# Performance work log

Hardware: AMD Instinct MI355X
Metric: run time of the kernel (lower is better)

The kernel has to match this reference:

```python
import jax, jax.numpy as jnp
import numpy as np

B, S, D_MODEL, D_MEM, N_HEADS, NU = 8, 2048, 1024, 1024, 16, 3
D_HEAD = D_MODEL // N_HEADS            # 64
D_KEY = 2 * NU * (D_MEM // N_HEADS)    # 384


def _to_heads(x, n_heads):
    b, s, d = x.shape
    return x.reshape(b, s, n_heads, d // n_heads).transpose(0, 2, 1, 3)


def _dpfp(x, nu):
    # Deterministic Positive Feature Projection: (..., d) -> (..., 2*nu*d)
    x = jnp.concatenate([jax.nn.relu(x), jax.nn.relu(-x)], axis=-1)
    rolled = jnp.concatenate([jnp.roll(x, j, axis=-1) for j in range(1, nu + 1)], axis=-1)
    rep = jnp.concatenate([x] * nu, axis=-1)
    return rep * rolled


def setup_inputs() -> dict:
    key = jax.random.key(0)
    k0, k1, k2, k3, k4 = jax.random.split(key, 5)
    mem_tokens = jax.random.normal(k0, (B, S, D_MODEL), dtype=jnp.float32)
    # nn.Linear(in, out) weight shape is [out, in]
    W_mk = jax.random.normal(k1, (D_MEM, D_MODEL), dtype=jnp.float32) * 0.02
    W_mv = jax.random.normal(k2, (D_MODEL, D_MODEL), dtype=jnp.float32) * 0.02
    W_mb = jax.random.normal(k3, (D_MODEL, D_MODEL), dtype=jnp.float32) * 0.02
    W_mem = jax.random.normal(k4, (B, N_HEADS, D_KEY, D_HEAD), dtype=jnp.float32) * 0.01
    z = jnp.ones((B, N_HEADS, D_KEY), dtype=jnp.float32)
    return {"mem_tokens": mem_tokens, "W_mk": W_mk, "W_mv": W_mv, "W_mb": W_mb,
            "W_mem": W_mem, "z": z}


def reference(mem_tokens, W_mk, W_mv, W_mb, W_mem, z):
    # key projection + DPFP feature map
    k = _to_heads(mem_tokens @ W_mk.T, N_HEADS)          # [b,h,s,d_mem/h]
    mk = _dpfp(k, NU)                                     # [b,h,s,d_key]
    norm = jnp.linalg.norm(mk, axis=-1, keepdims=True)
    mk = mk / jnp.maximum(norm, 1e-12)                    # F.normalize(p=2)

    new_mv = _to_heads(mem_tokens @ W_mv.T, N_HEADS)      # [b,h,s,d_head]

    # retrieve previous values (first_seg=False, use_denom=True path)
    num = jnp.einsum('bhsk,bhkd->bhsd', mk, W_mem)
    denom = jnp.einsum('bhk,bhsk->bhs', z, mk)[..., None] + 1e-5
    prev_mv = num / denom

    mv = new_mv - prev_mv
    mb = _to_heads(jax.nn.sigmoid(mem_tokens @ W_mb.T), N_HEADS)

    # gating=True einsum: 'ihjk,ihjt,ihjt->ihkt'
    associations = jnp.einsum('bhsk,bhsd,bhsd->bhkd', mk, mv, mb)
    return W_mem + associations
```

## Files before the change

kernel.cpp:

```cpp
#include <hip/hip_runtime.h>
#include <hip/hip_bf16.h>

#define B_ 8
#define S_ 2048
#define DM 1024
#define H_ 16
#define DH 64
#define DK 384

#define AS3 __attribute__((address_space(3)))
#define AS1 __attribute__((address_space(1)))
typedef unsigned int u32;

typedef __attribute__((ext_vector_type(8))) short bf16x8;
typedef __attribute__((ext_vector_type(4))) short bf16x4;
typedef __attribute__((ext_vector_type(4))) float f32x4;

static __device__ __forceinline__ ushort f2b(float f) {
  __hip_bfloat16 h = __float2bfloat16(f);
  return *reinterpret_cast<ushort*>(&h);
}
static __device__ __forceinline__ float b2f(ushort u) {
  __hip_bfloat16 h;
  *reinterpret_cast<ushort*>(&h) = u;
  return __bfloat162float(h);
}

__global__ __launch_bounds__(256) void k_cvt(
    const float* __restrict__ X, const float* __restrict__ Wk,
    const float* __restrict__ Wv, const float* __restrict__ Wb,
    ushort* __restrict__ Xb, ushort* __restrict__ Wball) {
  const int total = 2097152 + 3 * 131072;
  int c = blockIdx.x * 256 + threadIdx.x;
  const int stride = gridDim.x * 256;
  for (; c < total; c += stride) {
    const float* s;
    ushort* d;
    size_t off;
    if (c < 2097152) { s = X; d = Xb; off = (size_t)c; }
    else {
      int cc = c - 2097152;
      int wsel = cc >> 17;
      off = (size_t)(cc & 131071);
      s = wsel == 0 ? Wk : (wsel == 1 ? Wv : Wb);
      d = Wball + (size_t)wsel * (DM * DM);
    }
    float4 a = *(const float4*)(s + off * 8);
    float4 b = *(const float4*)(s + off * 8 + 4);
    ushort u[8] = { f2b(a.x), f2b(a.y), f2b(a.z), f2b(a.w),
                    f2b(b.x), f2b(b.y), f2b(b.z), f2b(b.w) };
    *(uint4*)(d + off * 8) = *(uint4*)u;
  }
}

__global__ __launch_bounds__(256) void k_proj(
    const ushort* __restrict__ Xb, const ushort* __restrict__ Wball,
    ushort* __restrict__ kvb) {
  __shared__ ushort SH[17408];
  ushort* As = SH;
  ushort* Bs = SH + 8192;
  const int t = threadIdx.x, lane = t & 63, w = t >> 6;
  const int wm = w >> 1, wn = w & 1;
  const int l15 = lane & 15, lq = lane >> 4;
  const int bid = blockIdx.x + (blockIdx.y << 7) + (blockIdx.z << 10);
  const int c = bid & 7, r = bid >> 3;
  const int zb = r >> 7;
  const int rem = r & 127;
  const int mgrp = rem >> 3;
  const int nb = rem & 7;
  const int m0 = (c * 16 + mgrp) * 128;
  const int n0 = nb * 128;
  const int wsel = zb;
  const ushort* Wmat = Wball + (size_t)wsel * (DM * DM);
  ushort* out = kvb + (size_t)wsel * ((size_t)B_ * H_ * S_ * DH);

  auto STAGE = [&](int buf, int k0) {
    #pragma unroll
    for (int j = 0; j < 2; j++) {
      int row = (t >> 2) + j * 64;
      int col8 = (t & 3) * 8;
      __builtin_amdgcn_global_load_lds(
          (const AS1 u32*)(Xb + (size_t)(m0 + row) * DM + k0 + col8),
          (AS3 u32*)(As + buf * 4096 + j * 2048 + t * 8), 16, 0, 0);
      __builtin_amdgcn_global_load_lds(
          (const AS1 u32*)(Wmat + (size_t)(n0 + row) * DM + k0 + col8),
          (AS3 u32*)(Bs + buf * 4096 + j * 2048 + t * 8), 16, 0, 0);
    }
  };

  f32x4 acc[4][4] = {};
  STAGE(0, 0);
  __syncthreads();
  int cur = 0;
  for (int kt = 0; kt < 32; kt++) {
    if (kt < 31) STAGE(cur ^ 1, (kt + 1) * 32);
    const ushort* Ab = As + cur * 4096;
    const ushort* Bb = Bs + cur * 4096;
    bf16x8 af[4], bfr[4];
    #pragma unroll
    for (int mi = 0; mi < 4; mi++)
      af[mi] = *(const bf16x8*)&Ab[(wm * 64 + mi * 16 + l15) * 32 + lq * 8];
    #pragma unroll
    for (int ni = 0; ni < 4; ni++)
      bfr[ni] = *(const bf16x8*)&Bb[(wn * 64 + ni * 16 + l15) * 32 + lq * 8];
    #pragma unroll
    for (int mi = 0; mi < 4; mi++)
      #pragma unroll
      for (int ni = 0; ni < 4; ni++)
        acc[mi][ni] = __builtin_amdgcn_mfma_f32_16x16x32_bf16(af[mi], bfr[ni], acc[mi][ni], 0, 0, 0);
    __syncthreads();
    cur ^= 1;
  }

  ushort (*Cb)[136] = (ushort (*)[136])SH;
  #pragma unroll
  for (int mi = 0; mi < 4; mi++)
    #pragma unroll
    for (int ni = 0; ni < 4; ni++)
      #pragma unroll
      for (int rr = 0; rr < 4; rr++) {
        float val = acc[mi][ni][rr];
        if (wsel == 2) val = 1.0f / (1.0f + __expf(-val));
        Cb[wm * 64 + mi * 16 + lq * 4 + rr][wn * 64 + ni * 16 + l15] = f2b(val);
      }
  __syncthreads();
  #pragma unroll
  for (int q = 0; q < 8; q++) {
    int idx = q * 256 + t;
    int lm = idx >> 4;
    int c16 = idx & 15;
    int m = m0 + lm;
    int b = m >> 11, s = m & 2047;
    int o0 = n0 + c16 * 8;
    int h = o0 >> 6, d = o0 & 63;
    *(uint4*)(out + (((size_t)(b * H_ + h)) * S_ + s) * DH + d) =
        *(uint4*)&Cb[lm][c16 * 8];
  }
}

__global__ __launch_bounds__(512) void k_fused6(
    const ushort* __restrict__ Kb, const ushort* __restrict__ Vb,
    const ushort* __restrict__ Bgb, const float* __restrict__ Wmem,
    const float* __restrict__ z, ushort* __restrict__ part) {
  __shared__ u32 mkLd[32][192];
  __shared__ ushort mkT[384][36];
  __shared__ ushort gLT[64][36];
  __shared__ ushort zL[384];
  const int t = threadIdx.x, l = t & 63, w = t >> 6;
  const int l15 = l & 15, lq = l >> 4;
  const int bh = blockIdx.y, seg = blockIdx.x;
  const size_t rowbase = (size_t)bh * S_;
  const int mi = w >> 2, ni = w & 3;
  const int dcol = ni * 16 + l15;

  for (int cc = t; cc < DK; cc += 512) {
    int u = cc >> 7, p = (cc & 127) >> 1, par = cc & 1;
    zL[cc] = f2b(z[(size_t)bh * DK + u * 128 + par * 64 + p]);
  }

  const float* Wm = Wmem + (size_t)bh * (DK * DH);
  bf16x8 bw[12];
  #pragma unroll
  for (int k0i = 0; k0i < 12; k0i++) {
    bf16x8 tmp;
    #pragma unroll
    for (int j = 0; j < 8; j++) {
      int cc = k0i * 32 + lq * 8 + j;
      int u = cc >> 7, p = (cc & 127) >> 1, par = cc & 1;
      tmp[j] = (short)f2b(Wm[(size_t)(u * 128 + par * 64 + p) * DH + dcol]);
    }
    bw[k0i] = tmp;
  }

  f32x4 acc[3][4] = {};
  ushort kreg[4], vreg[4], breg[4];

  auto LOADCH = [&](int ch) {
    const int s0 = seg * 512 + ch * 32;
    #pragma unroll
    for (int r = 0; r < 4; r++)
      kreg[r] = Kb[(rowbase + s0 + w * 4 + r) * DH + l];
    #pragma unroll
    for (int rr = 0; rr < 4; rr++) {
      size_t ga = (rowbase + s0 + mi * 16 + lq * 4 + rr) * DH + dcol;
      vreg[rr] = Vb[ga];
      breg[rr] = Bgb[ga];
    }
  };

  LOADCH(0);
  __syncthreads();

  for (int ch = 0; ch < 16; ch++) {
    float xpv[4], xnv[4];
    u32 pks[4];
    #pragma unroll
    for (int r = 0; r < 4; r++) {
      float kv = b2f(kreg[r]);
      xpv[r] = fmaxf(kv, 0.f);
      xnv[r] = fmaxf(-kv, 0.f);
      pks[r] = (u32)f2b(xpv[r]) | ((u32)f2b(xnv[r]) << 16);
    }
    ushort4 mp[6];
    #pragma unroll
    for (int u = 0; u < 3; u++) {
      int ie = (l - u - 1) & 127;
      int sl = ie & 63;
      bool sw = ie >= 64;
      #pragma unroll
      for (int r = 0; r < 4; r++) {
        u32 pp = (u32)__shfl((int)pks[r], sl);
        float ps = b2f((ushort)(pp & 0xffff));
        float ns = b2f((ushort)(pp >> 16));
        float xbe = sw ? ns : ps;
        float xbo = sw ? ps : ns;
        ushort bve = f2b(xpv[r] * xbe);
        ushort bvo = f2b(xnv[r] * xbo);
        int row = w * 4 + r;
        mkLd[row][(u * 64 + l) ^ ((row & 7) << 2)] = (u32)bve | ((u32)bvo << 16);
        ((ushort*)&mp[2 * u])[r] = bve;
        ((ushort*)&mp[2 * u + 1])[r] = bvo;
      }
    }
    #pragma unroll
    for (int tt = 0; tt < 6; tt++)
      *(ushort4*)&mkT[l + 64 * tt][w * 4] = mp[tt];
    __syncthreads();

    const u32* mkrow = &mkLd[mi * 16 + l15][0];
    const int xr = (l15 & 7) << 2;
    f32x4 an0 = {}, an1 = {}, gacc = {}, zacc = {};
    #pragma unroll
    for (int k0i = 0; k0i < 12; k0i += 2) {
      bf16x8 afA = *(const bf16x8*)(mkrow + ((k0i * 16 + lq * 4) ^ xr));
      bf16x8 afB = *(const bf16x8*)(mkrow + (((k0i + 1) * 16 + lq * 4) ^ xr));
      bf16x8 zfA = *(const bf16x8*)&zL[k0i * 32 + lq * 8];
      bf16x8 zfB = *(const bf16x8*)&zL[(k0i + 1) * 32 + lq * 8];
      an0 = __builtin_amdgcn_mfma_f32_16x16x32_bf16(afA, bw[k0i], an0, 0, 0, 0);
      an1 = __builtin_amdgcn_mfma_f32_16x16x32_bf16(afB, bw[k0i + 1], an1, 0, 0, 0);
      gacc = __builtin_amdgcn_mfma_f32_16x16x32_bf16(afA, afA, gacc, 0, 0, 0);
      gacc = __builtin_amdgcn_mfma_f32_16x16x32_bf16(afB, afB, gacc, 0, 0, 0);
      zacc = __builtin_amdgcn_mfma_f32_16x16x32_bf16(afA, zfA, zacc, 0, 0, 0);
      zacc = __builtin_amdgcn_mfma_f32_16x16x32_bf16(afB, zfB, zacc, 0, 0, 0);
    }
    f32x4 an = an0 + an1;
    float ssqv[4];
    #pragma unroll
    for (int rr = 0; rr < 4; rr++)
      ssqv[rr] = __shfl(gacc[rr], (lq << 4) + lq * 4 + rr);
    {
      ushort4 gp;
      #pragma unroll
      for (int rr = 0; rr < 4; rr++) {
        float inv = 1.0f / fmaxf(sqrtf(ssqv[rr]), 1e-12f);
        float rden = 1.0f / (inv * zacc[rr] + 1e-5f);
        float prev = an[rr] * inv * rden;
        float g = (b2f(vreg[rr]) - prev) * b2f(breg[rr]);
        ((ushort*)&gp)[rr] = f2b(g * inv);
      }
      *(ushort4*)&gLT[dcol][mi * 16 + lq * 4] = gp;
    }
    __syncthreads();

    if (ch < 15) LOADCH(ch + 1);

    {
      bf16x8 bfr[4];
      #pragma unroll
      for (int n2 = 0; n2 < 4; n2++) {
        bf16x4 blo = *(const bf16x4*)&gLT[n2 * 16 + l15][lq * 8];
        bf16x4 bhi = *(const bf16x4*)&gLT[n2 * 16 + l15][lq * 8 + 4];
        bfr[n2] = __builtin_shufflevector(blo, bhi, 0, 1, 2, 3, 4, 5, 6, 7);
      }
      #pragma unroll
      for (int m2 = 0; m2 < 3; m2++) {
        bf16x4 alo = *(const bf16x4*)&mkT[w * 48 + m2 * 16 + l15][lq * 8];
        bf16x4 ahi = *(const bf16x4*)&mkT[w * 48 + m2 * 16 + l15][lq * 8 + 4];
        bf16x8 af = __builtin_shufflevector(alo, ahi, 0, 1, 2, 3, 4, 5, 6, 7);
        #pragma unroll
        for (int n2 = 0; n2 < 4; n2++)
          acc[m2][n2] = __builtin_amdgcn_mfma_f32_16x16x32_bf16(af, bfr[n2], acc[m2][n2], 0, 0, 0);
      }
    }
    __syncthreads();
  }

  ushort* pb = part + ((size_t)bh * 4 + seg) * (DK * DH);
  #pragma unroll
  for (int m2 = 0; m2 < 3; m2++)
    #pragma unroll
    for (int n2 = 0; n2 < 4; n2++)
      #pragma unroll
      for (int rc = 0; rc < 4; rc++)
        pb[(size_t)(w * 48 + m2 * 16 + lq * 4 + rc) * DH + n2 * 16 + l15] =
            f2b(acc[m2][n2][rc]);
}

__global__ __launch_bounds__(256) void k_reduce(
    const float* __restrict__ Wmem, const ushort* __restrict__ part,
    float* __restrict__ out) {
  size_t i4 = (size_t)blockIdx.x * 256 + threadIdx.x;
  int bh = (int)(i4 / 6144);
  size_t r4 = i4 - (size_t)bh * 6144;
  float4 acc = *(const float4*)(Wmem + i4 * 4);
  #pragma unroll
  for (int k = 0; k < 4; k++) {
    const ushort* pp = part + ((size_t)bh * 4 + k) * (DK * DH) + r4 * 4;
    ushort4 pv = *(const ushort4*)pp;
    acc.x += b2f(pv.x);
    acc.y += b2f(pv.y);
    acc.z += b2f(pv.z);
    acc.w += b2f(pv.w);
  }
  *(float4*)(out + i4 * 4) = acc;
}

extern "C" void kernel_launch(void* const* d_in, const int* in_sizes, int n_in,
                              void* d_out, int out_size, void* d_ws, size_t ws_size,
                              hipStream_t stream) {
  const float* X  = (const float*)d_in[0];
  const float* Wk = (const float*)d_in[1];
  const float* Wv = (const float*)d_in[2];
  const float* Wb = (const float*)d_in[3];
  const float* Wm = (const float*)d_in[4];
  const float* z  = (const float*)d_in[5];
  float* out = (float*)d_out;
  char* ws = (char*)d_ws;

  ushort* Xb    = (ushort*)(ws);
  ushort* Wball = (ushort*)(ws + 33554432ull);
  ushort* kvb   = (ushort*)(ws + 39845888ull);
  ushort* part  = (ushort*)(ws);
  ushort* Kb  = kvb;
  ushort* Vb  = kvb + (size_t)B_ * H_ * S_ * DH;
  ushort* Bgb = kvb + 2ull * (size_t)B_ * H_ * S_ * DH;

  k_cvt   <<<dim3(2048), 256, 0, stream>>>(X, Wk, Wv, Wb, Xb, Wball);
  k_proj  <<<dim3(128, 8, 3), 256, 0, stream>>>(Xb, Wball, kvb);
  k_fused6<<<dim3(4, B_ * H_), 512, 0, stream>>>(Kb, Vb, Bgb, Wm, z, part);
  k_reduce<<<dim3(3072), 256, 0, stream>>>(Wm, part, out);
}
```

Baseline: 274.4 us.

## Double K-tile depth and XOR-swizzle LDS layout in projection GEMM

The projection GEMM now stages 64-wide K tiles instead of 32, halving the number of loop iterations and barriers. Global-to-LDS loads use an XOR swizzle on the 16-byte column chunks to avoid LDS bank conflicts on the fragment reads, and the row pointers are precomputed. The main loop is fully unrolled. LDS use grows to 64 KB per block, which may reduce occupancy.

```diff
diff --git a/kernel.cpp b/kernel.cpp
--- a/kernel.cpp
+++ b/kernel.cpp
@@ -56,9 +56,7 @@
 __global__ __launch_bounds__(256) void k_proj(
     const ushort* __restrict__ Xb, const ushort* __restrict__ Wball,
     ushort* __restrict__ kvb) {
-  __shared__ ushort SH[17408];
-  ushort* As = SH;
-  ushort* Bs = SH + 8192;
+  __shared__ ushort SH[4 * 8192];
   const int t = threadIdx.x, lane = t & 63, w = t >> 6;
   const int wm = w >> 1, wn = w & 1;
   const int l15 = lane & 15, lq = lane >> 4;
@@ -74,42 +72,62 @@
   const ushort* Wmat = Wball + (size_t)wsel * (DM * DM);
   ushort* out = kvb + (size_t)wsel * ((size_t)B_ * H_ * S_ * DH);
 
-  auto STAGE = [&](int buf, int k0) {
-    #pragma unroll
-    for (int j = 0; j < 2; j++) {
-      int row = (t >> 2) + j * 64;
-      int col8 = (t & 3) * 8;
+  const int rowst = (lane >> 3);
+  const int colsw = ((lane & 7) ^ rowst) << 3;
+
+  const ushort* pX[4];
+  const ushort* pW[4];
+  #pragma unroll
+  for (int j = 0; j < 4; j++) {
+    int row = (w * 4 + j) * 8 + rowst;
+    pX[j] = Xb + (size_t)(m0 + row) * DM + colsw;
+    pW[j] = Wmat + (size_t)(n0 + row) * DM + colsw;
+  }
+  ushort* dA = SH + w * 2048;
+  ushort* dB = SH + 16384 + w * 2048;
+
+  auto STAGE = [&](int buf, int kidx) {
+    #pragma unroll
+    for (int j = 0; j < 4; j++) {
       __builtin_amdgcn_global_load_lds(
-          (const AS1 u32*)(Xb + (size_t)(m0 + row) * DM + k0 + col8),
-          (AS3 u32*)(As + buf * 4096 + j * 2048 + t * 8), 16, 0, 0);
+          (const AS1 u32*)(pX[j] + kidx * 64),
+          (AS3 u32*)(dA + buf * 8192 + j * 512), 16, 0, 0);
       __builtin_amdgcn_global_load_lds(
-          (const AS1 u32*)(Wmat + (size_t)(n0 + row) * DM + k0 + col8),
-          (AS3 u32*)(Bs + buf * 4096 + j * 2048 + t * 8), 16, 0, 0);
+          (const AS1 u32*)(pW[j] + kidx * 64),
+          (AS3 u32*)(dB + buf * 8192 + j * 512), 16, 0, 0);
     }
   };
+
+  const int aoffb = (wm * 64 + l15) * 64;
+  const int boffb = (wn * 64 + l15) * 64;
+  const int csw0 = (lq ^ (lane & 7)) << 3;
+  const int csw1 = ((lq + 4) ^ (lane & 7)) << 3;
 
   f32x4 acc[4][4] = {};
   STAGE(0, 0);
   __syncthreads();
-  int cur = 0;
-  for (int kt = 0; kt < 32; kt++) {
-    if (kt < 31) STAGE(cur ^ 1, (kt + 1) * 32);
-    const ushort* Ab = As + cur * 4096;
-    const ushort* Bb = Bs + cur * 4096;
-    bf16x8 af[4], bfr[4];
-    #pragma unroll
-    for (int mi = 0; mi < 4; mi++)
-      af[mi] = *(const bf16x8*)&Ab[(wm * 64 + mi * 16 + l15) * 32 + lq * 8];
-    #pragma unroll
-    for (int ni = 0; ni < 4; ni++)
-      bfr[ni] = *(const bf16x8*)&Bb[(wn * 64 + ni * 16 + l15) * 32 + lq * 8];
-    #pragma unroll
-    for (int mi = 0; mi < 4; mi++)
+  #pragma unroll
+  for (int kt = 0; kt < 16; kt++) {
+    const int cur = kt & 1;
+    if (kt < 15) STAGE(cur ^ 1, kt + 1);
+    const int ab = cur * 8192;
+    #pragma unroll
+    for (int kk2 = 0; kk2 < 2; kk2++) {
+      const int csw = kk2 ? csw1 : csw0;
+      bf16x8 af[4], bfr[4];
+      #pragma unroll
+      for (int mi = 0; mi < 4; mi++)
+        af[mi] = *(const bf16x8*)&SH[ab + aoffb + mi * 1024 + csw];
       #pragma unroll
       for (int ni = 0; ni < 4; ni++)
-        acc[mi][ni] = __builtin_amdgcn_mfma_f32_16x16x32_bf16(af[mi], bfr[ni], acc[mi][ni], 0, 0, 0);
+        bfr[ni] = *(const bf16x8*)&SH[16384 + ab + boffb + ni * 1024 + csw];
+      #pragma unroll
+      for (int mi = 0; mi < 4; mi++)
+        #pragma unroll
+        for (int ni = 0; ni < 4; ni++)
+          acc[mi][ni] = __builtin_amdgcn_mfma_f32_16x16x32_bf16(af[mi], bfr[ni], acc[mi][ni], 0, 0, 0);
+    }
     __syncthreads();
-    cur ^= 1;
   }
 
   ushort (*Cb)[136] = (ushort (*)[136])SH;
```

Result: faster. 245.8 us (-10.4%).
